# Performance work log

Measured on AMD Instinct MI355X. Metric: run time of the kernel, lower is better.

Reference implementation:

```python
import jax, jax.numpy as jnp
import numpy as np

D, E, DFF, TOPK = 768, 4, 1024, 2


def setup_inputs() -> dict:
    key = jax.random.key(0)
    ks = jax.random.split(key, 6)
    s = 0.02  # init scale for weights
    return {
        "input_ids": jax.random.normal(ks[0], (8, 2048, D), dtype=jnp.float32),
        "W": jax.random.normal(ks[1], (D, D), dtype=jnp.float32) * s,
        "b": jnp.zeros((D,), dtype=jnp.float32),
        "Wg": jax.random.normal(ks[2], (D, E), dtype=jnp.float32) * s,
        "bg": jnp.zeros((E,), dtype=jnp.float32),
        "W1": jax.random.normal(ks[3], (E, D, DFF), dtype=jnp.float32) * s,
        "b1": jnp.zeros((E, DFF), dtype=jnp.float32),
        "W2": jax.random.normal(ks[4], (E, DFF, D), dtype=jnp.float32) * s,
        "b2": jnp.zeros((E, D), dtype=jnp.float32),
    }


def reference(input_ids, W, b, Wg, bg, W1, b1, W2, b2):
    B, S, _ = input_ids.shape
    # Dense projection feeding the MoE layer
    h = jnp.einsum("bsd,de->bse", input_ids, W) + b          # [B,S,D]
    t = h.reshape(-1, D)                                      # [T,D] tokens

    # Token-choice router: softmax over experts, top-2, renormalized gates
    logits = t @ Wg + bg                                      # [T,E]
    probs = jax.nn.softmax(logits, axis=-1)
    vals, idx = jax.lax.top_k(probs, TOPK)                    # [T,K]
    gates = vals / jnp.sum(vals, axis=-1, keepdims=True)
    # Dense combine weights [T,E]: zero for non-selected experts
    comb = jnp.sum(jax.nn.one_hot(idx, E, dtype=t.dtype) * gates[..., None], axis=1)

    # Expert FFNs (E small -> compute all experts, weighted combine)
    pre = jnp.einsum("td,edf->etf", t, W1) + b1[:, None, :]   # [E,T,DFF]
    y_e = jnp.einsum("etf,efd->etd", jax.nn.gelu(pre), W2) + b2[:, None, :]
    out = jnp.einsum("te,etd->td", comb, y_e)                 # [T,D]
    return out.reshape(B, S, D)
```

## Files before the change

### kernel.cpp

```cpp
#include <hip/hip_runtime.h>

#define DIM 768
#define NEXP 4
#define DFF_ 1024
#define CAP 16384

typedef __attribute__((ext_vector_type(4))) float f32x4;
typedef __attribute__((ext_vector_type(8))) short s16x8;

__device__ __forceinline__ unsigned short f32_to_bf16(float f) {
  unsigned int u = __float_as_uint(f);
  unsigned int r = (u + 0x7FFFu + ((u >> 16) & 1u)) >> 16;
  return (unsigned short)r;
}
__device__ __forceinline__ float bf16_to_f32(unsigned short u) {
  return __uint_as_float(((unsigned int)u) << 16);
}
__device__ __forceinline__ unsigned lds_off(const void* p) {
  return (unsigned)(unsigned long long)(__attribute__((address_space(3))) const void*)p;
}

__global__ void transpose_bf16_kernel(const float* __restrict__ in,
                                      unsigned short* __restrict__ out,
                                      int R, int C, int ldo, int zOut) {
  __shared__ float tile[32][33];
  const int bx = blockIdx.x, by = blockIdx.y, bz = blockIdx.z;
  in  += (size_t)bz * R * C;
  out += (size_t)bz * zOut;
  const int tx = threadIdx.x, ty = threadIdx.y;
#pragma unroll
  for (int i = 0; i < 4; i++) {
    int r = by * 32 + ty + i * 8;
    int c = bx * 32 + tx;
    tile[ty + i * 8][tx] = in[(size_t)r * C + c];
  }
  __syncthreads();
#pragma unroll
  for (int i = 0; i < 4; i++) {
    int oc = bx * 32 + ty + i * 8;
    int orow = by * 32 + tx;
    out[(size_t)oc * ldo + orow] = f32_to_bf16(tile[tx][ty + i * 8]);
  }
}

__global__ void wfg_kernel(const float* __restrict__ W, const float* __restrict__ Wg,
                           const float* __restrict__ b, const float* __restrict__ bg,
                           float* __restrict__ wfg, float* __restrict__ bgp) {
  int gid = blockIdx.x * 256 + threadIdx.x;
  if (gid < DIM * NEXP) {
    int k = gid >> 2, e = gid & 3;
    const float* wr = W + (size_t)k * DIM;
    float acc = 0.f;
    for (int d = 0; d < DIM; d++) acc += wr[d] * Wg[d * NEXP + e];
    wfg[gid] = acc;
  } else if (gid < DIM * NEXP + NEXP) {
    int e = gid - DIM * NEXP;
    float acc = bg[e];
    for (int d = 0; d < DIM; d++) acc += b[d] * Wg[d * NEXP + e];
    bgp[e] = acc;
  }
}

__global__ void router_kernel(const float* __restrict__ x, const float* __restrict__ wfg,
                              const float* __restrict__ bgp,
                              int2* __restrict__ rte, float2* __restrict__ rtg,
                              unsigned short* __restrict__ xbf) {
  __shared__ float wfgS[DIM * NEXP];
  const int tid = threadIdx.x;
  for (int i = tid; i < DIM * NEXP; i += 256) wfgS[i] = wfg[i];
  __syncthreads();
  const int w = tid >> 6, lane = tid & 63;
  const size_t t = (size_t)blockIdx.x * 4 + w;
  const float* xr = x + t * DIM;
  unsigned short* xbr = xbf + t * DIM;
  float a0 = 0.f, a1 = 0.f, a2 = 0.f, a3 = 0.f;
#pragma unroll
  for (int i = 0; i < 6; i++) {
    int k = i * 128 + lane * 2;
    float2 xv = *(const float2*)(xr + k);
    ushort2 pk;
    pk.x = f32_to_bf16(xv.x);
    pk.y = f32_to_bf16(xv.y);
    *(ushort2*)(xbr + k) = pk;
    a0 += xv.x * wfgS[k * 4 + 0] + xv.y * wfgS[k * 4 + 4];
    a1 += xv.x * wfgS[k * 4 + 1] + xv.y * wfgS[k * 4 + 5];
    a2 += xv.x * wfgS[k * 4 + 2] + xv.y * wfgS[k * 4 + 6];
    a3 += xv.x * wfgS[k * 4 + 3] + xv.y * wfgS[k * 4 + 7];
  }
#pragma unroll
  for (int off = 32; off > 0; off >>= 1) {
    a0 += __shfl_xor(a0, off);
    a1 += __shfl_xor(a1, off);
    a2 += __shfl_xor(a2, off);
    a3 += __shfl_xor(a3, off);
  }
  if (lane == 0) {
    float l[NEXP] = {a0 + bgp[0], a1 + bgp[1], a2 + bgp[2], a3 + bgp[3]};
    float m = fmaxf(fmaxf(l[0], l[1]), fmaxf(l[2], l[3]));
    float p[NEXP]; float s = 0.f;
#pragma unroll
    for (int e = 0; e < NEXP; e++) { p[e] = expf(l[e] - m); s += p[e]; }
#pragma unroll
    for (int e = 0; e < NEXP; e++) p[e] /= s;
    int i1 = 0;
#pragma unroll
    for (int e = 1; e < NEXP; e++) if (p[e] > p[i1]) i1 = e;
    int i2 = -1;
#pragma unroll
    for (int e = 0; e < NEXP; e++) { if (e == i1) continue; if (i2 < 0 || p[e] > p[i2]) i2 = e; }
    float denom = p[i1] + p[i2];
    rte[t] = make_int2(i1, i2);
    rtg[t] = make_float2(p[i1] / denom, p[i2] / denom);
  }
}

__global__ void assign_kernel(const int2* __restrict__ rte, const float2* __restrict__ rtg,
                              int* __restrict__ cnt, int* __restrict__ idx_tok,
                              float* __restrict__ gate_sel, int2* __restrict__ tok_slot) {
  __shared__ int hist[NEXP];
  __shared__ int base[NEXP];
  const int tid = threadIdx.x;
  if (tid < NEXP) hist[tid] = 0;
  __syncthreads();
  const int t = blockIdx.x * 256 + tid;
  int2 e = rte[t];
  float2 g = rtg[t];
  int r1 = atomicAdd(&hist[e.x], 1);
  int r2 = atomicAdd(&hist[e.y], 1);
  __syncthreads();
  if (tid < NEXP) base[tid] = atomicAdd(&cnt[tid], hist[tid]);
  __syncthreads();
  int s1 = base[e.x] + r1, s2 = base[e.y] + r2;
  idx_tok[e.x * CAP + s1] = t;  gate_sel[e.x * CAP + s1] = g.x;
  idx_tok[e.y * CAP + s2] = t;  gate_sel[e.y * CAP + s2] = g.y;
  tok_slot[t] = make_int2((e.x << 14) | s1, (e.y << 14) | s2);
}

__global__ void combine_kernel(const unsigned short* __restrict__ y,
                               const int2* __restrict__ tok_slot,
                               const float2* __restrict__ rtg,
                               const int* __restrict__ cnts,
                               const float* __restrict__ b2,
                               float* __restrict__ out) {
  __shared__ float b2S[NEXP * DIM];
  const int tid = threadIdx.x;
  for (int i = tid; i < NEXP * DIM; i += 256) b2S[i] = b2[i];
  const int t0 = (cnts[0] + 127) >> 7, t1 = (cnts[1] + 127) >> 7, t2 = (cnts[2] + 127) >> 7;
  const int rb[NEXP] = {0, t0 * 128, (t0 + t1) * 128, (t0 + t1 + t2) * 128};
  __syncthreads();
  const int w = tid >> 6, lane = tid & 63;
  const size_t t = (size_t)blockIdx.x * 4 + w;
  int2 v = tok_slot[t];
  float2 cg = rtg[t];
  const int e1 = v.x >> 14, s1 = v.x & (CAP - 1);
  const int e2 = v.y >> 14, s2 = v.y & (CAP - 1);
  const unsigned short* y1 = y + (size_t)(rb[e1] + s1) * DIM;
  const unsigned short* y2 = y + (size_t)(rb[e2] + s2) * DIM;
  float* op = out + t * DIM;
  const float* bp1 = b2S + e1 * DIM;
  const float* bp2 = b2S + e2 * DIM;
#pragma unroll
  for (int k = 0; k < 12; k++) {
    int n = k * 64 + lane;
    op[n] = bf16_to_f32(y1[n]) + bf16_to_f32(y2[n]) + cg.x * bp1[n] + cg.y * bp2[n];
  }
}

template <int MODE, int CH, int NT>
__launch_bounds__(256, 3)
__global__ void gemm_kernel(const unsigned short* __restrict__ A, const int lda,
                            const unsigned short* __restrict__ Bt, const int ldb,
                            const int N,
                            const float* __restrict__ bias,
                            const int* __restrict__ idx_tok,
                            const float* __restrict__ gate_sel,
                            const int* __restrict__ cnts,
                            unsigned short* __restrict__ outB, const int ldo) {
  const int lin = blockIdx.y * gridDim.x + blockIdx.x;
  const int nT = gridDim.x;
  const int xcd = lin & 7, t8 = lin >> 3;
  int bn = 0, bm0 = 0;
  int bmLoc = 0, cnt = 1 << 30, segBase = 0, gRow0 = 0;

  if constexpr (MODE == 0) {
    const int perXcd = gridDim.y >> 3;
    const int mi = t8 % CH;
    const int rest = t8 / CH;
    bn = rest % nT;
    const int mc = rest / nT;
    bm0 = (xcd * perXcd + mc * CH + mi) * 128;
  } else {
    const int c0 = cnts[0], c1 = cnts[1], c2 = cnts[2], c3 = cnts[3];
    const int t0 = (c0 + 127) >> 7, t1 = (c1 + 127) >> 7,
              t2 = (c2 + 127) >> 7, t3 = (c3 + 127) >> 7;
    const int p1 = t0, p2 = p1 + t1, p3 = p2 + t2, tot = p3 + t3;
    const int perXcd = (tot + 7) >> 3;
    bn = t8 % nT;
    const int mloc = t8 / nT;
    if (mloc >= perXcd) return;
    const int mIdx = xcd * perXcd + mloc;
    if (mIdx >= tot) return;
    const int seg = (mIdx >= p2) ? ((mIdx >= p3) ? 3 : 2) : ((mIdx >= p1) ? 1 : 0);
    const int pre = (seg == 3) ? p3 : (seg == 2) ? p2 : (seg == 1) ? p1 : 0;
    bmLoc = (mIdx - pre) * 128;
    segBase = seg * CAP;
    gRow0 = mIdx * 128;
    cnt = (seg == 3) ? c3 : (seg == 2) ? c2 : (seg == 1) ? c1 : c0;
    Bt += (size_t)seg * N * ldb;
    if constexpr (MODE == 1) bias += (size_t)seg * N;
  }

  __shared__ unsigned short As[3][128 * 32];
  __shared__ unsigned short Bs[3][128 * 32];
  __shared__ int idxS[128];
  __shared__ float gateS[128];

  const int tid = threadIdx.x;
  const int w = tid >> 6;
  const int lane = tid & 63;

  if constexpr (MODE == 1) {
    if (tid < 128) {
      int r = bmLoc + tid;
      int cl = (r < cnt) ? r : bmLoc;
      idxS[tid] = idx_tok[segBase + cl];
      gateS[tid] = gate_sel[segBase + cl];
    }
    __syncthreads();
  }

  const int r0 = tid >> 2, r1 = 64 + r0;
  const int gq = (tid & 3) ^ (r0 & 3);
  const unsigned short *aP0, *aP1;
  if constexpr (MODE == 0) {
    aP0 = A + (size_t)(bm0 + r0) * lda + gq * 8;
    aP1 = A + (size_t)(bm0 + r1) * lda + gq * 8;
  } else if constexpr (MODE == 1) {
    aP0 = A + (size_t)idxS[r0] * lda + gq * 8;
    aP1 = A + (size_t)idxS[r1] * lda + gq * 8;
  } else {
    aP0 = A + (size_t)(gRow0 + r0) * lda + gq * 8;
    aP1 = A + (size_t)(gRow0 + r1) * lda + gq * 8;
  }
  const unsigned short* bP0 = Bt + (size_t)(bn * 128 + r0) * ldb + gq * 8;
  const unsigned short* bP1 = Bt + (size_t)(bn * 128 + r1) * ldb + gq * 8;

  const int quad = lane >> 4;
  const int m16 = lane & 15;
  const int wm = (w & 1) * 64;
  const int wn = (w >> 1) * 64;
  const int sw = (quad ^ (m16 & 3)) * 16;

  const unsigned aBase0 = lds_off(&As[0][0]);
  const unsigned bBase0 = lds_off(&Bs[0][0]);
  const unsigned aRd = (unsigned)((wm + m16) * 64 + sw);
  const unsigned bRd = (unsigned)((wn + m16) * 64 + sw);

  f32x4 acc[4][4];
#pragma unroll
  for (int i = 0; i < 4; i++)
#pragma unroll
    for (int j = 0; j < 4; j++) acc[i][j] = (f32x4){0.f, 0.f, 0.f, 0.f};

#define GLL(src, dst)                                                              \
  __builtin_amdgcn_global_load_lds((const __attribute__((address_space(1))) void*)(src), \
                                   (__attribute__((address_space(3))) void*)(dst), 16, 0, 0)
#define ISSUE(off, kk)                                                   \
  {                                                                      \
    char* la0 = (char*)&As[0][0] + (off) + w * 1024;                     \
    char* lb0 = (char*)&Bs[0][0] + (off) + w * 1024;                     \
    GLL(aP0 + (kk), la0);                                                \
    GLL(aP1 + (kk), la0 + 4096);                                         \
    GLL(bP0 + (kk), lb0);                                                \
    GLL(bP1 + (kk), lb0 + 4096);                                         \
  }
#define DSR(dst, addr, imm) \
  asm volatile("ds_read_b128 %0, %1 offset:" #imm : "=v"(dst) : "v"(addr))
#define KSTEP(GATE)                                                          \
  {                                                                          \
    asm volatile("s_waitcnt vmcnt(" #GATE ")" ::: "memory");                 \
    __builtin_amdgcn_s_barrier();                                            \
    asm volatile("" ::: "memory");                                           \
    s16x8 af[4], bf4[4];                                                     \
    const unsigned aAd = aBase0 + curOff + aRd;                              \
    const unsigned bAd = bBase0 + curOff + bRd;                              \
    DSR(af[0], aAd, 0);                                                      \
    DSR(af[1], aAd, 1024);                                                   \
    DSR(af[2], aAd, 2048);                                                   \
    DSR(af[3], aAd, 3072);                                                   \
    DSR(bf4[0], bAd, 0);                                                     \
    DSR(bf4[1], bAd, 1024);                                                  \
    DSR(bf4[2], bAd, 2048);                                                  \
    DSR(bf4[3], bAd, 3072);                                                  \
    asm volatile("s_waitcnt lgkmcnt(0)" ::: "memory");                       \
    __builtin_amdgcn_sched_barrier(0);                                       \
    __builtin_amdgcn_s_barrier();                                            \
    asm volatile("" ::: "memory");                                           \
    __builtin_amdgcn_s_setprio(1);                                           \
    _Pragma("unroll") for (int i_ = 0; i_ < 4; i_++)                         \
    _Pragma("unroll") for (int j_ = 0; j_ < 4; j_++)                         \
      acc[i_][j_] = __builtin_amdgcn_mfma_f32_16x16x32_bf16(af[i_], bf4[j_], \
                                                            acc[i_][j_], 0, 0, 0); \
    __builtin_amdgcn_s_setprio(0);                                           \
    curOff = (curOff == 16384u) ? 0u : curOff + 8192u;                       \
  }

  ISSUE(0, 0);
  ISSUE(8192, 32);
  unsigned curOff = 0;
  unsigned stOff = 16384;
  int kk = 64;

  static_assert(NT >= 3, "NT must be >= 3");
#pragma unroll 1
  for (int i = 0; i < NT - 2; ++i) {
    ISSUE(stOff, kk);
    kk += 32;
    stOff = (stOff == 16384u) ? 0u : stOff + 8192u;
    KSTEP(8);
  }
  KSTEP(4);
  KSTEP(0);

#undef KSTEP
#undef DSR
#undef ISSUE
#undef GLL

#pragma unroll
  for (int i = 0; i < 4; i++) {
    const int rloc = wm + i * 16 + quad * 4;
#pragma unroll
    for (int j = 0; j < 4; j++) {
      const int col = bn * 128 + wn + j * 16 + m16;
      if constexpr (MODE == 0) {
        float bv = bias[col];
#pragma unroll
        for (int r = 0; r < 4; r++)
          outB[(size_t)(bm0 + rloc + r) * ldo + col] = f32_to_bf16(acc[i][j][r] + bv);
      } else if constexpr (MODE == 1) {
        float bv = bias[col];
#pragma unroll
        for (int r = 0; r < 4; r++) {
          if (bmLoc + rloc + r < cnt) {
            float v = acc[i][j][r] + bv;
            float t3 = v + 0.044715f * v * v * v;
            float e2 = exp2f(t3 * 2.302208206984525f);
            float rc = __builtin_amdgcn_rcpf(1.0f + e2);
            float g = v - v * rc;
            outB[(size_t)(gRow0 + rloc + r) * ldo + col] = f32_to_bf16(g * gateS[rloc + r]);
          }
        }
      } else {
#pragma unroll
        for (int r = 0; r < 4; r++) {
          if (bmLoc + rloc + r < cnt)
            outB[(size_t)(gRow0 + rloc + r) * ldo + col] = f32_to_bf16(acc[i][j][r]);
        }
      }
    }
  }
}

extern "C" void kernel_launch(void* const* d_in, const int* in_sizes, int n_in,
                              void* d_out, int out_size, void* d_ws, size_t ws_size,
                              hipStream_t stream) {
  (void)in_sizes; (void)n_in; (void)out_size; (void)ws_size;
  const float* x  = (const float*)d_in[0];
  const float* W  = (const float*)d_in[1];
  const float* b  = (const float*)d_in[2];
  const float* Wg = (const float*)d_in[3];
  const float* bg = (const float*)d_in[4];
  const float* W1 = (const float*)d_in[5];
  const float* b1 = (const float*)d_in[6];
  const float* W2 = (const float*)d_in[7];
  const float* b2 = (const float*)d_in[8];
  float* out = (float*)d_out;
  char* ws = (char*)d_ws;

  unsigned short* tbf  = (unsigned short*)(ws + 0);
  unsigned short* w1t  = (unsigned short*)(ws + 25165824);
  unsigned short* w2t  = (unsigned short*)(ws + 31457280);
  float* wfg           = (float*)(ws + 37748736);
  float* bgp           = (float*)(ws + 37761024);
  int2*  rte           = (int2*)(ws + 37761280);
  float2* rtg          = (float2*)(ws + 37892352);
  int*   cnt           = (int*)(ws + 38023424);
  int*   idx_tok       = (int*)(ws + 38023680);
  float* gate_sel      = (float*)(ws + 38285824);
  int2*  tok_slot      = (int2*)(ws + 38547968);
  unsigned short* g    = (unsigned short*)(ws + 38679040);
  unsigned short* xbf  = (unsigned short*)(ws + 38679040);
  unsigned short* wt   = (unsigned short*)(ws + 63844864);
  unsigned short* y    = (unsigned short*)(ws + 106574336);

  hipMemsetAsync(cnt, 0, NEXP * sizeof(int), stream);
  transpose_bf16_kernel<<<dim3(24, 24, 1), dim3(32, 8), 0, stream>>>(W, wt, 768, 768, 768, 589824);
  transpose_bf16_kernel<<<dim3(32, 24, 4), dim3(32, 8), 0, stream>>>(W1, w1t, 768, 1024, 768, 786432);
  transpose_bf16_kernel<<<dim3(24, 32, 4), dim3(32, 8), 0, stream>>>(W2, w2t, 1024, 768, 1024, 786432);
  wfg_kernel<<<13, 256, 0, stream>>>(W, Wg, b, bg, wfg, bgp);
  router_kernel<<<4096, 256, 0, stream>>>(x, wfg, bgp, rte, rtg, xbf);
  assign_kernel<<<64, 256, 0, stream>>>(rte, rtg, cnt, idx_tok, gate_sel, tok_slot);

  gemm_kernel<0, 8, 24><<<dim3(6, 128), 256, 0, stream>>>(
      xbf, 768, wt, 768, 768, b, nullptr, nullptr, nullptr, tbf, 768);
  gemm_kernel<1, 8, 24><<<dim3(8, 264), 256, 0, stream>>>(
      tbf, 768, w1t, 768, 1024, b1, idx_tok, gate_sel, cnt, g, 1024);
  gemm_kernel<2, 8, 32><<<dim3(6, 264), 256, 0, stream>>>(
      g, 1024, w2t, 1024, 768, nullptr, nullptr, nullptr, cnt, y, 768);
  combine_kernel<<<4096, 256, 0, stream>>>(y, tok_slot, rtg, cnt, b2, out);
}
```

Baseline: 397.6 us.

## Pre-pack weights into MFMA fragment layout and load B directly to registers

Replaces the weight transpose with a pack kernel that writes each 16-column by 32-k tile in the exact per-lane order the MFMA B operand expects. The GEMM then loads B fragments straight from global memory into registers with double-buffered global_load_dwordx4, dropping the B LDS tiles and their ds_reads. This halves LDS traffic and footprint, at the cost of more VGPRs and B loads that each wave issues for itself with no sharing through LDS. The K loop is unrolled by two to alternate register sets, and NT must now be even.

```diff
diff --git a/kernel.cpp b/kernel.cpp
--- a/kernel.cpp
+++ b/kernel.cpp
@@ -20,27 +20,23 @@
   return (unsigned)(unsigned long long)(__attribute__((address_space(3))) const void*)p;
 }
 
-__global__ void transpose_bf16_kernel(const float* __restrict__ in,
-                                      unsigned short* __restrict__ out,
-                                      int R, int C, int ldo, int zOut) {
-  __shared__ float tile[32][33];
-  const int bx = blockIdx.x, by = blockIdx.y, bz = blockIdx.z;
-  in  += (size_t)bz * R * C;
-  out += (size_t)bz * zOut;
-  const int tx = threadIdx.x, ty = threadIdx.y;
-#pragma unroll
-  for (int i = 0; i < 4; i++) {
-    int r = by * 32 + ty + i * 8;
-    int c = bx * 32 + tx;
-    tile[ty + i * 8][tx] = in[(size_t)r * C + c];
-  }
-  __syncthreads();
-#pragma unroll
-  for (int i = 0; i < 4; i++) {
-    int oc = bx * 32 + ty + i * 8;
-    int orow = by * 32 + tx;
-    out[(size_t)oc * ldo + orow] = f32_to_bf16(tile[tx][ty + i * 8]);
-  }
+__global__ void pack_bf16_kernel(const float* __restrict__ in,
+                                 unsigned short* __restrict__ out,
+                                 int K, int C) {
+  const int t = threadIdx.x;
+  const int lane = t & 63;
+  const int pb = blockIdx.x * 4 + (t >> 6);
+  const int KT = K >> 5;
+  const int n16 = pb / KT, kt = pb - n16 * KT;
+  const int z = blockIdx.z;
+  in  += (size_t)z * K * C;
+  out += (size_t)z * K * C;
+  const int col = n16 * 16 + (lane & 15);
+  const int k0 = kt * 32 + (lane >> 4) * 8;
+  s16x8 vv;
+#pragma unroll
+  for (int e = 0; e < 8; e++) vv[e] = (short)f32_to_bf16(in[(size_t)(k0 + e) * C + col]);
+  *(s16x8*)(out + (size_t)pb * 512 + lane * 8) = vv;
 }
 
 __global__ void wfg_kernel(const float* __restrict__ W, const float* __restrict__ Wg,
@@ -169,7 +165,7 @@
 template <int MODE, int CH, int NT>
 __launch_bounds__(256, 3)
 __global__ void gemm_kernel(const unsigned short* __restrict__ A, const int lda,
-                            const unsigned short* __restrict__ Bt, const int ldb,
+                            const unsigned short* __restrict__ Bp, const int ldb,
                             const int N,
                             const float* __restrict__ bias,
                             const int* __restrict__ idx_tok,
@@ -181,6 +177,7 @@
   const int xcd = lin & 7, t8 = lin >> 3;
   int bn = 0, bm0 = 0;
   int bmLoc = 0, cnt = 1 << 30, segBase = 0, gRow0 = 0;
+  const unsigned short* Bt = Bp;
 
   if constexpr (MODE == 0) {
     const int perXcd = gridDim.y >> 3;
@@ -211,7 +208,6 @@
   }
 
   __shared__ unsigned short As[3][128 * 32];
-  __shared__ unsigned short Bs[3][128 * 32];
   __shared__ int idxS[128];
   __shared__ float gateS[128];
 
@@ -242,8 +238,6 @@
     aP0 = A + (size_t)(gRow0 + r0) * lda + gq * 8;
     aP1 = A + (size_t)(gRow0 + r1) * lda + gq * 8;
   }
-  const unsigned short* bP0 = Bt + (size_t)(bn * 128 + r0) * ldb + gq * 8;
-  const unsigned short* bP1 = Bt + (size_t)(bn * 128 + r1) * ldb + gq * 8;
 
   const int quad = lane >> 4;
   const int m16 = lane & 15;
@@ -252,46 +246,52 @@
   const int sw = (quad ^ (m16 & 3)) * 16;
 
   const unsigned aBase0 = lds_off(&As[0][0]);
-  const unsigned bBase0 = lds_off(&Bs[0][0]);
   const unsigned aRd = (unsigned)((wm + m16) * 64 + sw);
-  const unsigned bRd = (unsigned)((wn + m16) * 64 + sw);
+
+  const unsigned short* bp0 = Bt + (size_t)(bn * 8 + (w >> 1) * 4 + 0) * NT * 512 + lane * 8;
+  const unsigned short* bp1 = Bt + (size_t)(bn * 8 + (w >> 1) * 4 + 1) * NT * 512 + lane * 8;
+  const unsigned short* bp2 = Bt + (size_t)(bn * 8 + (w >> 1) * 4 + 2) * NT * 512 + lane * 8;
+  const unsigned short* bp3 = Bt + (size_t)(bn * 8 + (w >> 1) * 4 + 3) * NT * 512 + lane * 8;
 
   f32x4 acc[4][4];
 #pragma unroll
   for (int i = 0; i < 4; i++)
 #pragma unroll
     for (int j = 0; j < 4; j++) acc[i][j] = (f32x4){0.f, 0.f, 0.f, 0.f};
+
+  s16x8 br0[4], br1[4];
 
 #define GLL(src, dst)                                                              \
   __builtin_amdgcn_global_load_lds((const __attribute__((address_space(1))) void*)(src), \
                                    (__attribute__((address_space(3))) void*)(dst), 16, 0, 0)
-#define ISSUE(off, kk)                                                   \
+#define ISSUE_A(off, kk)                                                 \
   {                                                                      \
     char* la0 = (char*)&As[0][0] + (off) + w * 1024;                     \
-    char* lb0 = (char*)&Bs[0][0] + (off) + w * 1024;                     \
     GLL(aP0 + (kk), la0);                                                \
     GLL(aP1 + (kk), la0 + 4096);                                         \
-    GLL(bP0 + (kk), lb0);                                                \
-    GLL(bP1 + (kk), lb0 + 4096);                                         \
+  }
+#define LOADB(SET)                                                                   \
+  {                                                                                  \
+    asm volatile("global_load_dwordx4 %0, %1, off" : "=v"(br##SET[0]) : "v"(bp0));   \
+    asm volatile("global_load_dwordx4 %0, %1, off" : "=v"(br##SET[1]) : "v"(bp1));   \
+    asm volatile("global_load_dwordx4 %0, %1, off" : "=v"(br##SET[2]) : "v"(bp2));   \
+    asm volatile("global_load_dwordx4 %0, %1, off" : "=v"(br##SET[3]) : "v"(bp3));   \
+    bp0 += 512; bp1 += 512; bp2 += 512; bp3 += 512;                                  \
   }
 #define DSR(dst, addr, imm) \
   asm volatile("ds_read_b128 %0, %1 offset:" #imm : "=v"(dst) : "v"(addr))
-#define KSTEP(GATE)                                                          \
+#define KSTEP(GATE, SET)                                                     \
   {                                                                          \
     asm volatile("s_waitcnt vmcnt(" #GATE ")" ::: "memory");                 \
+    __builtin_amdgcn_sched_barrier(0);                                       \
     __builtin_amdgcn_s_barrier();                                            \
     asm volatile("" ::: "memory");                                           \
-    s16x8 af[4], bf4[4];                                                     \
+    s16x8 af[4];                                                             \
     const unsigned aAd = aBase0 + curOff + aRd;                              \
-    const unsigned bAd = bBase0 + curOff + bRd;                              \
     DSR(af[0], aAd, 0);                                                      \
     DSR(af[1], aAd, 1024);                                                   \
     DSR(af[2], aAd, 2048);                                                   \
     DSR(af[3], aAd, 3072);                                                   \
-    DSR(bf4[0], bAd, 0);                                                     \
-    DSR(bf4[1], bAd, 1024);                                                  \
-    DSR(bf4[2], bAd, 2048);                                                  \
-    DSR(bf4[3], bAd, 3072);                                                  \
     asm volatile("s_waitcnt lgkmcnt(0)" ::: "memory");                       \
     __builtin_amdgcn_sched_barrier(0);                                       \
     __builtin_amdgcn_s_barrier();                                            \
@@ -299,32 +299,41 @@
     __builtin_amdgcn_s_setprio(1);                                           \
     _Pragma("unroll") for (int i_ = 0; i_ < 4; i_++)                         \
     _Pragma("unroll") for (int j_ = 0; j_ < 4; j_++)                         \
-      acc[i_][j_] = __builtin_amdgcn_mfma_f32_16x16x32_bf16(af[i_], bf4[j_], \
+      acc[i_][j_] = __builtin_amdgcn_mfma_f32_16x16x32_bf16(af[i_], br##SET[j_], \
                                                             acc[i_][j_], 0, 0, 0); \
     __builtin_amdgcn_s_setprio(0);                                           \
     curOff = (curOff == 16384u) ? 0u : curOff + 8192u;                       \
   }
 
-  ISSUE(0, 0);
-  ISSUE(8192, 32);
+  ISSUE_A(0, 0);
+  LOADB(0);
+  ISSUE_A(8192, 32);
   unsigned curOff = 0;
   unsigned stOff = 16384;
   int kk = 64;
 
-  static_assert(NT >= 3, "NT must be >= 3");
+  static_assert(NT >= 4 && (NT & 1) == 0, "NT must be even, >= 4");
 #pragma unroll 1
-  for (int i = 0; i < NT - 2; ++i) {
-    ISSUE(stOff, kk);
+  for (int ii = 0; ii < (NT - 2) / 2; ii++) {
+    LOADB(1);
+    ISSUE_A(stOff, kk);
     kk += 32;
     stOff = (stOff == 16384u) ? 0u : stOff + 8192u;
-    KSTEP(8);
-  }
-  KSTEP(4);
-  KSTEP(0);
+    KSTEP(8, 0);
+    LOADB(0);
+    ISSUE_A(stOff, kk);
+    kk += 32;
+    stOff = (stOff == 16384u) ? 0u : stOff + 8192u;
+    KSTEP(8, 1);
+  }
+  LOADB(1);
+  KSTEP(6, 0);
+  KSTEP(0, 1);
 
 #undef KSTEP
 #undef DSR
-#undef ISSUE
+#undef LOADB
+#undef ISSUE_A
 #undef GLL
 
 #pragma unroll
@@ -379,8 +388,8 @@
   char* ws = (char*)d_ws;
 
   unsigned short* tbf  = (unsigned short*)(ws + 0);
-  unsigned short* w1t  = (unsigned short*)(ws + 25165824);
-  unsigned short* w2t  = (unsigned short*)(ws + 31457280);
+  unsigned short* w1p  = (unsigned short*)(ws + 25165824);
+  unsigned short* w2p  = (unsigned short*)(ws + 31457280);
   float* wfg           = (float*)(ws + 37748736);
   float* bgp           = (float*)(ws + 37761024);
   int2*  rte           = (int2*)(ws + 37761280);
@@ -391,22 +400,22 @@
   int2*  tok_slot      = (int2*)(ws + 38547968);
   unsigned short* g    = (unsigned short*)(ws + 38679040);
   unsigned short* xbf  = (unsigned short*)(ws + 38679040);
-  unsigned short* wt   = (unsigned short*)(ws + 63844864);
+  unsigned short* wp   = (unsigned short*)(ws + 63844864);
   unsigned short* y    = (unsigned short*)(ws + 106574336);
 
   hipMemsetAsync(cnt, 0, NEXP * sizeof(int), stream);
-  transpose_bf16_kernel<<<dim3(24, 24, 1), dim3(32, 8), 0, stream>>>(W, wt, 768, 768, 768, 589824);
-  transpose_bf16_kernel<<<dim3(32, 24, 4), dim3(32, 8), 0, stream>>>(W1, w1t, 768, 1024, 768, 786432);
-  transpose_bf16_kernel<<<dim3(24, 32, 4), dim3(32, 8), 0, stream>>>(W2, w2t, 1024, 768, 1024, 786432);
+  pack_bf16_kernel<<<dim3(288, 1, 1), 256, 0, stream>>>(W, wp, 768, 768);
+  pack_bf16_kernel<<<dim3(384, 1, 4), 256, 0, stream>>>(W1, w1p, 768, 1024);
+  pack_bf16_kernel<<<dim3(384, 1, 4), 256, 0, stream>>>(W2, w2p, 1024, 768);
   wfg_kernel<<<13, 256, 0, stream>>>(W, Wg, b, bg, wfg, bgp);
   router_kernel<<<4096, 256, 0, stream>>>(x, wfg, bgp, rte, rtg, xbf);
   assign_kernel<<<64, 256, 0, stream>>>(rte, rtg, cnt, idx_tok, gate_sel, tok_slot);
 
   gemm_kernel<0, 8, 24><<<dim3(6, 128), 256, 0, stream>>>(
-      xbf, 768, wt, 768, 768, b, nullptr, nullptr, nullptr, tbf, 768);
+      xbf, 768, wp, 768, 768, b, nullptr, nullptr, nullptr, tbf, 768);
   gemm_kernel<1, 8, 24><<<dim3(8, 264), 256, 0, stream>>>(
-      tbf, 768, w1t, 768, 1024, b1, idx_tok, gate_sel, cnt, g, 1024);
+      tbf, 768, w1p, 768, 1024, b1, idx_tok, gate_sel, cnt, g, 1024);
   gemm_kernel<2, 8, 32><<<dim3(6, 264), 256, 0, stream>>>(
-      g, 1024, w2t, 1024, 768, nullptr, nullptr, nullptr, cnt, y, 768);
+      g, 1024, w2p, 1024, 768, nullptr, nullptr, nullptr, cnt, y, 768);
   combine_kernel<<<4096, 256, 0, stream>>>(y, tok_slot, rtg, cnt, b2, out);
 }
```

Result: faster. 376.7 us (-5.2%).
